# Performance work log

Hardware: AMD Instinct MI355X
Metric: run time of the kernel (lower is better)

## Reference

```python
import jax, jax.numpy as jnp
import numpy as np

B, N = 512, 256
NODE_D = 256      # inpt_dim[1]
PE_D = 256        # pooled_edge_dim
GLOB_D = 64       # inpt_dim[2]
FEAT_IN = NODE_D + PE_D          # 512, LN dim
CTXT_IN = GLOB_D                 # ctxt_dim = 0
FEAT_OUT = 256                   # feat_kwargs.outp_dim
N_HEADS = 4                      # attn_kwargs.outp_dim
HEAD_DIM = FEAT_OUT // N_HEADS   # 64
FEAT_HID = 1024
ATTN_HID = 256
LN_EPS = 1e-5


def _mlp(x, w1, b1, w2, b2):
    # DenseNetwork: hidden layer with SiLU, linear output
    h = jax.nn.silu(jnp.einsum('bni,ih->bnh', x, w1) + b1)
    return jnp.einsum('bnh,ho->bno', h, w2) + b2


def setup_inputs() -> dict:
    key = jax.random.key(0)
    ks = jax.random.split(key, 12)
    s = lambda fan_in: 1.0 / np.sqrt(fan_in)
    mask = jax.random.randint(ks[2], (B, N), 0, 2).astype(bool)
    mask = mask.at[:, 0].set(True)  # guarantee >=1 valid node per graph
    return {
        'nodes': jax.random.normal(ks[0], (B, N, NODE_D), jnp.float32),
        'pooled_edges': jax.random.normal(ks[1], (B, N, PE_D), jnp.float32),
        'mask': mask,
        'globs': jax.random.normal(ks[3], (B, GLOB_D), jnp.float32),
        'ln_g': jnp.ones((FEAT_IN,), jnp.float32),
        'ln_b': jnp.zeros((FEAT_IN,), jnp.float32),
        'fw1': jax.random.normal(ks[4], (FEAT_IN + CTXT_IN, FEAT_HID), jnp.float32) * s(FEAT_IN + CTXT_IN),
        'fb1': jnp.zeros((FEAT_HID,), jnp.float32),
        'fw2': jax.random.normal(ks[5], (FEAT_HID, FEAT_OUT), jnp.float32) * s(FEAT_HID),
        'fb2': jnp.zeros((FEAT_OUT,), jnp.float32),
        'aw1': jax.random.normal(ks[6], (FEAT_IN + CTXT_IN, ATTN_HID), jnp.float32) * s(FEAT_IN + CTXT_IN),
        'ab1': jnp.zeros((ATTN_HID,), jnp.float32),
        'aw2': jax.random.normal(ks[7], (ATTN_HID, N_HEADS), jnp.float32) * s(ATTN_HID),
        'ab2': jnp.zeros((N_HEADS,), jnp.float32),
    }


def reference(nodes, pooled_edges, mask, globs, ln_g, ln_b,
              fw1, fb1, fw2, fb2, aw1, ab1, aw2, ab2):
    # concat node feats with pooled edge feats, pre-LN
    x = jnp.concatenate([nodes, pooled_edges], axis=-1)            # [B,N,512]
    mu = jnp.mean(x, axis=-1, keepdims=True)
    var = jnp.mean(jnp.square(x - mu), axis=-1, keepdims=True)
    xn = (x - mu) * jax.lax.rsqrt(var + LN_EPS) * ln_g + ln_b
    # high-level context (globals) broadcast to every node
    ctx = jnp.broadcast_to(globs[:, None, :], (B, N, GLOB_D))
    inp = jnp.concatenate([xn, ctx], axis=-1)                      # [B,N,576]
    # attention pooling weights: pass_with_mask with padval=-inf, softmax over nodes
    scores = _mlp(inp, aw1, ab1, aw2, ab2)                         # [B,N,H]
    scores = jnp.where(mask[..., None], scores, -jnp.inf)
    w = jax.nn.softmax(scores / np.sqrt(FEAT_OUT).astype(np.float32), axis=-2)
    w = jnp.nan_to_num(w)                                          # all-masked graphs -> 0
    pool_w = jnp.repeat(w, HEAD_DIM, axis=-1)                      # [B,N,H*head_dim]
    # feature net: pass_with_mask with padval=0
    feats = _mlp(inp, fw1, fb1, fw2, fb2)                          # [B,N,256]
    feats = jnp.where(mask[..., None], feats, 0.0)
    # additive residual
    new_nodes = feats + nodes
    # attention pooled global
    pooled = jnp.sum(new_nodes * pool_w, axis=-2)                  # [B,256]
    return new_nodes, pooled
```

## Files before the change

### kernel.cpp

```cpp
#include <hip/hip_runtime.h>
#include <cmath>

typedef unsigned short ushort_t;
typedef unsigned char uchar_t;
typedef short short8 __attribute__((ext_vector_type(8)));
typedef float floatx4 __attribute__((ext_vector_type(4)));

#define B_GRAPH 512
#define ROWS 131072
#define IN_D 576
#define FEAT_HID 1024
#define ATTN_HID 256
#define NCAT 1280
#define FEAT_OUT 256
#define BK 32
#define NBUF 3
#define TILE_ELEMS (128 * BK)
#define BUF_BYTES  (TILE_ELEMS * 2)

__device__ __forceinline__ float bf2f(ushort_t h) {
    return __uint_as_float(((unsigned int)h) << 16);
}
__device__ __forceinline__ ushort_t f2bf(float f) {
    unsigned int u = __float_as_uint(f);
    u += 0x7fffu + ((u >> 16) & 1u);
    return (ushort_t)(u >> 16);
}
__device__ __forceinline__ void load4bf(const ushort_t* p, float f[4]) {
    uint2 u = *(const uint2*)p;
    f[0] = __uint_as_float(u.x << 16);
    f[1] = __uint_as_float(u.x & 0xffff0000u);
    f[2] = __uint_as_float(u.y << 16);
    f[3] = __uint_as_float(u.y & 0xffff0000u);
}

__global__ void detect_kernel(const void* nodes, const void* maskp, int* flags) {
    const int t = threadIdx.x;
    const ushort_t* nb = (const ushort_t*)nodes;
    int cnt = 0;
    for (int i = t; i < 4096; i += 256) {
        unsigned e = ((unsigned)nb[i] >> 7) & 0xffu;
        if (e >= 147u) cnt++;
    }
    const unsigned* mw = (const unsigned*)maskp;
    int mcnt = 0;
    for (int i = t; i < 16384; i += 256) {
        if (mw[i] > 1u) mcnt++;
    }
    __shared__ int r1[256], r2[256];
    r1[t] = cnt; r2[t] = mcnt; __syncthreads();
    for (int off = 128; off > 0; off >>= 1) {
        if (t < off) { r1[t] += r1[t + off]; r2[t] += r2[t + off]; }
        __syncthreads();
    }
    if (t == 0) { flags[0] = (r1[0] > 64) ? 1 : 0; flags[1] = (r2[0] > 16) ? 1 : 0; }
}

__device__ __forceinline__ float loadany(const void* p, size_t i, int flag) {
    return flag ? ((const float*)p)[i] : bf2f(((const ushort_t*)p)[i]);
}
__device__ __forceinline__ bool maskany(const void* p, size_t i, int flagM) {
    return flagM ? (((const uchar_t*)p)[i] != 0) : (((const int*)p)[i] != 0);
}

__global__ __launch_bounds__(256)
void convert_all(const void* globs, const void* lng, const void* lnb,
                 const void* fb1, const void* fb2, const void* ab1, const void* ab2,
                 ushort_t* gcan, ushort_t* lgc, ushort_t* lbc,
                 ushort_t* bcat, ushort_t* fb2c, ushort_t* ab2c,
                 const int* flags) {
    const int flag = flags[0];
    int i = blockIdx.x * 256 + threadIdx.x;
    if (i < 32768) { gcan[i] = f2bf(loadany(globs, i, flag)); return; }
    i -= 32768;
    if (i < 512)   { lgc[i]  = f2bf(loadany(lng,   i, flag)); return; }
    i -= 512;
    if (i < 512)   { lbc[i]  = f2bf(loadany(lnb,   i, flag)); return; }
    i -= 512;
    if (i < 1024)  { bcat[i] = f2bf(loadany(fb1,   i, flag)); return; }
    i -= 1024;
    if (i < 256)   { bcat[1024 + i] = f2bf(loadany(ab1, i, flag)); return; }
    i -= 256;
    if (i < 256)   { fb2c[i] = f2bf(loadany(fb2,   i, flag)); return; }
    i -= 256;
    if (i < 4)     { ab2c[i] = f2bf(loadany(ab2,   i, flag)); }
}

__global__ __launch_bounds__(256)
void transpose_all(const void* fw1, const void* fw2, const void* aw1, const void* aw2,
                   ushort_t* w1cat, ushort_t* fw2t, ushort_t* aw2t,
                   const int* flags) {
    const int flag = flags[0];
    int i = blockIdx.x * 256 + threadIdx.x;
    if (i < 576 * 1024) {
        int r = i >> 10, c = i & 1023;
        w1cat[(size_t)c * 576 + r] = f2bf(loadany(fw1, i, flag)); return;
    }
    i -= 576 * 1024;
    if (i < 1024 * 256) {
        int r = i >> 8, c = i & 255;
        fw2t[(size_t)c * 1024 + r] = f2bf(loadany(fw2, i, flag)); return;
    }
    i -= 1024 * 256;
    if (i < 576 * 256) {
        int r = i >> 8, c = i & 255;
        w1cat[(size_t)(1024 + c) * 576 + r] = f2bf(loadany(aw1, i, flag)); return;
    }
    i -= 576 * 256;
    if (i < 256 * 4) {
        int r = i >> 2, c = i & 3;
        aw2t[(size_t)c * 256 + r] = f2bf(loadany(aw2, i, flag));
    }
}

__global__ __launch_bounds__(256)
void ln_concat_kernel(const void* __restrict__ nodes, const void* __restrict__ pe,
                      const ushort_t* __restrict__ gcan,
                      const ushort_t* __restrict__ lg, const ushort_t* __restrict__ lb,
                      ushort_t* __restrict__ inp, int row0, const int* __restrict__ flags) {
    const int flag = flags[0];
    const int row  = blockIdx.x * 4 + (threadIdx.x >> 6);
    const int lane = threadIdx.x & 63;
    const size_t grow = (size_t)row0 + row;
    float xa[4], xb[4];
    if (flag) {
        float4 a = *(const float4*)((const float*)nodes + grow * 256 + lane * 4);
        float4 b = *(const float4*)((const float*)pe    + grow * 256 + lane * 4);
        xa[0]=a.x; xa[1]=a.y; xa[2]=a.z; xa[3]=a.w;
        xb[0]=b.x; xb[1]=b.y; xb[2]=b.z; xb[3]=b.w;
    } else {
        load4bf((const ushort_t*)nodes + grow * 256 + lane * 4, xa);
        load4bf((const ushort_t*)pe    + grow * 256 + lane * 4, xb);
    }
    float s = 0.f, q = 0.f;
#pragma unroll
    for (int j = 0; j < 4; j++) { s += xa[j] + xb[j]; q += xa[j]*xa[j] + xb[j]*xb[j]; }
#pragma unroll
    for (int m = 1; m < 64; m <<= 1) { s += __shfl_xor(s, m, 64); q += __shfl_xor(q, m, 64); }
    const float mu   = s * (1.0f / 512.0f);
    const float var  = q * (1.0f / 512.0f) - mu * mu;
    const float rstd = rsqrtf(fmaxf(var, 0.f) + 1e-5f);
    float ga[4], gb[4], ba[4], bb[4];
    load4bf(lg + lane * 4, ga);  load4bf(lg + 256 + lane * 4, gb);
    load4bf(lb + lane * 4, ba);  load4bf(lb + 256 + lane * 4, bb);
    ushort_t r0[4], r1[4];
#pragma unroll
    for (int j = 0; j < 4; j++) {
        r0[j] = f2bf((xa[j] - mu) * rstd * ga[j] + ba[j]);
        r1[j] = f2bf((xb[j] - mu) * rstd * gb[j] + bb[j]);
    }
    ushort_t* op = inp + (size_t)row * IN_D;
    uint2 p0, p1;
    p0.x = (unsigned)r0[0] | ((unsigned)r0[1] << 16);
    p0.y = (unsigned)r0[2] | ((unsigned)r0[3] << 16);
    p1.x = (unsigned)r1[0] | ((unsigned)r1[1] << 16);
    p1.y = (unsigned)r1[2] | ((unsigned)r1[3] << 16);
    *(uint2*)(op + lane * 4)       = p0;
    *(uint2*)(op + 256 + lane * 4) = p1;
    op[512 + lane] = gcan[(grow >> 8) * 64 + lane];
}

struct GemmCore {
    floatx4 acc[4][4];
    int wm, wn, r16, quad;
};

__device__ __forceinline__ void gload16(const ushort_t* g, ushort_t* l) {
    __builtin_amdgcn_global_load_lds(
        (const __attribute__((address_space(1))) unsigned int*)g,
        (__attribute__((address_space(3))) unsigned int*)l, 16, 0, 0);
}
__device__ __forceinline__ unsigned lds_off(const void* p) {
    return (unsigned)(size_t)(const __attribute__((address_space(3))) char*)p;
}

__device__ __forceinline__ void gemm_core(GemmCore& g,
        const ushort_t* __restrict__ A, int lda, const ushort_t* __restrict__ Bt,
        int m0, int n0, int K, ushort_t* As, ushort_t* Bs) {
    const int tid = threadIdx.x;
    const int wave = tid >> 6, lane = tid & 63;
    g.wm = (wave >> 1) * 64; g.wn = (wave & 1) * 64;
    g.r16 = lane & 15; g.quad = lane >> 4;
#pragma unroll
    for (int i = 0; i < 4; i++)
#pragma unroll
        for (int j = 0; j < 4; j++) g.acc[i][j] = (floatx4){0.f, 0.f, 0.f, 0.f};

    const int srow = wave * 32 + (lane >> 2);
    const int scol = (lane & 3) * 8;
    const ushort_t* Ag = A + (size_t)(m0 + srow) * lda + scol;
    const ushort_t* Bg = Bt + (size_t)(n0 + srow) * K + scol;
    const int woff = wave * 32 * BK;

    const unsigned a_lane = lds_off(As) + (unsigned)(((g.wm + g.r16) * BK + g.quad * 8) * 2);
    const unsigned b_lane = lds_off(Bs) + (unsigned)(((g.wn + g.r16) * BK + g.quad * 8) * 2);

    const int NT = K / BK;
    gload16(Ag, As + woff);
    gload16(Ag + 16 * (size_t)lda, As + woff + 16 * BK);
    gload16(Bg, Bs + woff);
    gload16(Bg + 16 * (size_t)K,  Bs + woff + 16 * BK);
    if (NT > 1) {
        gload16(Ag + BK, As + TILE_ELEMS + woff);
        gload16(Ag + BK + 16 * (size_t)lda, As + TILE_ELEMS + woff + 16 * BK);
        gload16(Bg + BK, Bs + TILE_ELEMS + woff);
        gload16(Bg + BK + 16 * (size_t)K,  Bs + TILE_ELEMS + woff + 16 * BK);
    }
    int bufc = 0;
    for (int t = 0; t < NT; ++t) {
        if (t + 1 < NT) asm volatile("s_waitcnt vmcnt(4)" ::: "memory");
        else            asm volatile("s_waitcnt vmcnt(0)" ::: "memory");
        __builtin_amdgcn_s_barrier();
        if (t + 2 < NT) {
            int bn = bufc + 2; if (bn >= NBUF) bn -= NBUF;
            const size_t kb = (size_t)(t + 2) * BK;
            ushort_t* An = As + bn * TILE_ELEMS + woff;
            ushort_t* Bn = Bs + bn * TILE_ELEMS + woff;
            gload16(Ag + kb, An);
            gload16(Ag + kb + 16 * (size_t)lda, An + 16 * BK);
            gload16(Bg + kb, Bn);
            gload16(Bg + kb + 16 * (size_t)K,  Bn + 16 * BK);
        }
        const unsigned aaddr = a_lane + (unsigned)(bufc * BUF_BYTES);
        const unsigned baddr = b_lane + (unsigned)(bufc * BUF_BYTES);
        short8 af[4], bg[4];
#pragma unroll
        for (int i = 0; i < 4; i++)
            asm volatile("ds_read_b128 %0, %1 offset:%c2"
                         : "=v"(af[i]) : "v"(aaddr), "i"(i * 1024));
#pragma unroll
        for (int i = 0; i < 4; i++)
            asm volatile("ds_read_b128 %0, %1 offset:%c2"
                         : "=v"(bg[i]) : "v"(baddr), "i"(i * 1024));
        asm volatile("s_waitcnt lgkmcnt(0)" ::: "memory");
        __builtin_amdgcn_sched_barrier(0);
#pragma unroll
        for (int mi = 0; mi < 4; mi++)
#pragma unroll
            for (int ni = 0; ni < 4; ni++)
                g.acc[mi][ni] = __builtin_amdgcn_mfma_f32_16x16x32_bf16(
                    af[mi], bg[ni], g.acc[mi][ni], 0, 0, 0);
        bufc = bufc + 1 == NBUF ? 0 : bufc + 1;
    }
}

__global__ __launch_bounds__(256)
void gemm_silu(const ushort_t* __restrict__ A, int lda,
               const ushort_t* __restrict__ Bt,
               const ushort_t* __restrict__ bias, ushort_t* __restrict__ out,
               int N, int K) {
    __shared__ __align__(16) ushort_t As[NBUF * TILE_ELEMS];
    __shared__ __align__(16) ushort_t Bs[NBUF * TILE_ELEMS];
    const int m0 = blockIdx.x * 128, n0 = blockIdx.y * 128;
    GemmCore g;
    gemm_core(g, A, lda, Bt, m0, n0, K, As, Bs);
#pragma unroll
    for (int mi = 0; mi < 4; mi++) {
        const int rbase = m0 + g.wm + mi * 16 + g.quad * 4;
#pragma unroll
        for (int ni = 0; ni < 4; ni++) {
            const int col = n0 + g.wn + ni * 16 + g.r16;
            const float bv = bf2f(bias[col]);
#pragma unroll
            for (int r = 0; r < 4; r++) {
                float v = g.acc[mi][ni][r] + bv;
                v = v / (1.0f + expf(-v));
                out[(size_t)(rbase + r) * N + col] = f2bf(v);
            }
        }
    }
}

__global__ __launch_bounds__(256)
void gemm_out(const ushort_t* __restrict__ A, int lda,
              const ushort_t* __restrict__ Bt,
              const ushort_t* __restrict__ bias, void* __restrict__ out,
              const void* __restrict__ mask, const void* __restrict__ resid,
              int row0, int K, const int* __restrict__ flags) {
    __shared__ __align__(16) ushort_t As[NBUF * TILE_ELEMS];
    __shared__ __align__(16) ushort_t Bs[NBUF * TILE_ELEMS];
    const int flag = flags[0], flagM = flags[1];
    const int m0 = blockIdx.x * 128, n0 = blockIdx.y * 128;
    GemmCore g;
    gemm_core(g, A, lda, Bt, m0, n0, K, As, Bs);
#pragma unroll
    for (int mi = 0; mi < 4; mi++) {
        const int rbase = m0 + g.wm + mi * 16 + g.quad * 4;
#pragma unroll
        for (int ni = 0; ni < 4; ni++) {
            const int col = n0 + g.wn + ni * 16 + g.r16;
            const float bv = bf2f(bias[col]);
#pragma unroll
            for (int r = 0; r < 4; r++) {
                const size_t grow = (size_t)row0 + rbase + r;
                const float nd = loadany(resid, grow * FEAT_OUT + col, flag);
                const bool mk = maskany(mask, grow, flagM);
                float v = mk ? (g.acc[mi][ni][r] + bv + nd) : nd;
                if (flag) ((float*)out)[grow * FEAT_OUT + col] = v;
                else      ((ushort_t*)out)[grow * FEAT_OUT + col] = f2bf(v);
            }
        }
    }
}

__global__ __launch_bounds__(256)
void scores_kernel(const ushort_t* __restrict__ hcat,
                   const ushort_t* __restrict__ aw2t,
                   const ushort_t* __restrict__ ab2c,
                   float* __restrict__ scores, int row0) {
    const int row  = blockIdx.x * 4 + (threadIdx.x >> 6);
    const int lane = threadIdx.x & 63;
    float x[4];
    load4bf(hcat + (size_t)row * NCAT + 1024 + lane * 4, x);
    float acc[4];
#pragma unroll
    for (int h = 0; h < 4; h++) {
        float wv[4];
        load4bf(aw2t + h * 256 + lane * 4, wv);
        acc[h] = x[0]*wv[0] + x[1]*wv[1] + x[2]*wv[2] + x[3]*wv[3];
    }
#pragma unroll
    for (int m = 1; m < 64; m <<= 1)
#pragma unroll
        for (int h = 0; h < 4; h++) acc[h] += __shfl_xor(acc[h], m, 64);
    if (lane == 0) {
#pragma unroll
        for (int h = 0; h < 4; h++)
            scores[((size_t)row0 + row) * 4 + h] = acc[h] + bf2f(ab2c[h]);
    }
}

__global__ __launch_bounds__(256)
void softmax_kernel(const float* __restrict__ scores, const void* __restrict__ mask,
                    float* __restrict__ w, const int* __restrict__ flags) {
    const int flagM = flags[1];
    const int b = blockIdx.x, n = threadIdx.x;
    const int idx = b * 256 + n;
    float4 s = *(const float4*)(scores + (size_t)idx * 4);
    s.x *= 0.0625f; s.y *= 0.0625f; s.z *= 0.0625f; s.w *= 0.0625f;
    const bool mk = maskany(mask, idx, flagM);
    __shared__ float4 red[256];
    float4 v;
    v.x = mk ? s.x : -3.0e38f; v.y = mk ? s.y : -3.0e38f;
    v.z = mk ? s.z : -3.0e38f; v.w = mk ? s.w : -3.0e38f;
    red[n] = v; __syncthreads();
    for (int off = 128; off > 0; off >>= 1) {
        if (n < off) {
            float4 o = red[n + off], c = red[n];
            c.x = fmaxf(c.x, o.x); c.y = fmaxf(c.y, o.y);
            c.z = fmaxf(c.z, o.z); c.w = fmaxf(c.w, o.w);
            red[n] = c;
        }
        __syncthreads();
    }
    float4 mx = red[0]; __syncthreads();
    float4 e;
    e.x = mk ? expf(s.x - mx.x) : 0.f; e.y = mk ? expf(s.y - mx.y) : 0.f;
    e.z = mk ? expf(s.z - mx.z) : 0.f; e.w = mk ? expf(s.w - mx.w) : 0.f;
    red[n] = e; __syncthreads();
    for (int off = 128; off > 0; off >>= 1) {
        if (n < off) {
            float4 o = red[n + off], c = red[n];
            c.x += o.x; c.y += o.y; c.z += o.z; c.w += o.w;
            red[n] = c;
        }
        __syncthreads();
    }
    float4 sm = red[0];
    const float ix = (sm.x > 0.f) ? 1.f / sm.x : 0.f;
    const float iy = (sm.y > 0.f) ? 1.f / sm.y : 0.f;
    const float iz = (sm.z > 0.f) ? 1.f / sm.z : 0.f;
    const float iw = (sm.w > 0.f) ? 1.f / sm.w : 0.f;
    float4 r; r.x = e.x * ix; r.y = e.y * iy; r.z = e.z * iz; r.w = e.w * iw;
    *(float4*)(w + (size_t)idx * 4) = r;
}

__global__ __launch_bounds__(256)
void pooled_kernel(const void* __restrict__ dout, const float* __restrict__ w,
                   const int* __restrict__ flags) {
    const int flag = flags[0];
    const int b = blockIdx.x, t = threadIdx.x;
    __shared__ float wsh[1024];
    const float* wb = w + (size_t)b * 1024;
    for (int i = t; i < 1024; i += 256) wsh[i] = wb[i];
    __syncthreads();
    const int h = t >> 6;
    float acc = 0.f;
    const size_t base = (size_t)b * 65536;
    if (flag) {
        const float* nn = (const float*)dout + base;
#pragma unroll 4
        for (int n = 0; n < 256; n++) acc += nn[(size_t)n * 256 + t] * wsh[n * 4 + h];
        ((float*)dout)[(size_t)ROWS * 256 + (size_t)b * 256 + t] = acc;
    } else {
        const ushort_t* nn = (const ushort_t*)dout + base;
#pragma unroll 4
        for (int n = 0; n < 256; n++) acc += bf2f(nn[(size_t)n * 256 + t]) * wsh[n * 4 + h];
        ((ushort_t*)dout)[(size_t)ROWS * 256 + (size_t)b * 256 + t] = f2bf(acc);
    }
}

extern "C" void kernel_launch(void* const* d_in, const int* in_sizes, int n_in,
                              void* d_out, int out_size, void* d_ws, size_t ws_size,
                              hipStream_t stream) {
    (void)in_sizes; (void)n_in; (void)out_size;
    const void* nodes = d_in[0];
    const void* pe    = d_in[1];
    const void* mask  = d_in[2];
    const void* globs = d_in[3];
    const void* ln_g  = d_in[4];
    const void* ln_b  = d_in[5];
    const void* fw1   = d_in[6];
    const void* fb1   = d_in[7];
    const void* fw2   = d_in[8];
    const void* fb2   = d_in[9];
    const void* aw1   = d_in[10];
    const void* ab1   = d_in[11];
    const void* aw2   = d_in[12];
    const void* ab2   = d_in[13];

    const int CHR = (ws_size >= (size_t)80 * 1024 * 1024) ? 16384 : 8192;

    char* ws = (char*)d_ws;
    size_t o = 0;
    auto take = [&](size_t bytes) -> char* {
        char* p = ws + o;
        o += (bytes + 255) & ~(size_t)255;
        return p;
    };
    ushort_t* inp  = (ushort_t*)take((size_t)CHR * IN_D * 2);
    ushort_t* hcat = (ushort_t*)take((size_t)CHR * NCAT * 2);
    float*    sc   = (float*)   take((size_t)ROWS * 4 * 4);
    float*    wsm  = (float*)   take((size_t)ROWS * 4 * 4);
    ushort_t* w1cat= (ushort_t*)take((size_t)NCAT * 576 * 2);
    ushort_t* fw2t = (ushort_t*)take(1024 * 256 * 2);
    ushort_t* aw2t = (ushort_t*)take(256 * 4 * 2);
    ushort_t* gcan = (ushort_t*)take(32768 * 2);
    ushort_t* lgc  = (ushort_t*)take(512 * 2);
    ushort_t* lbc  = (ushort_t*)take(512 * 2);
    ushort_t* bcat = (ushort_t*)take((size_t)NCAT * 2);
    ushort_t* fb2c = (ushort_t*)take(256 * 2);
    ushort_t* ab2c = (ushort_t*)take(4 * 2);
    int*      flags= (int*)     take(64);

    detect_kernel<<<1, 256, 0, stream>>>(nodes, mask, flags);
    convert_all<<<139, 256, 0, stream>>>(globs, ln_g, ln_b, fb1, fb2, ab1, ab2,
                                         gcan, lgc, lbc, bcat, fb2c, ab2c, flags);
    transpose_all<<<3908, 256, 0, stream>>>(fw1, fw2, aw1, aw2,
                                            w1cat, fw2t, aw2t, flags);

    const int nchunk = ROWS / CHR;
    for (int c = 0; c < nchunk; c++) {
        const int row0 = c * CHR;
        ln_concat_kernel<<<CHR / 4, 256, 0, stream>>>(nodes, pe, gcan, lgc, lbc,
                                                      inp, row0, flags);
        gemm_silu<<<dim3(CHR / 128, NCAT / 128), 256, 0, stream>>>(
            inp, IN_D, w1cat, bcat, hcat, NCAT, IN_D);
        scores_kernel<<<CHR / 4, 256, 0, stream>>>(hcat, aw2t, ab2c, sc, row0);
        gemm_out<<<dim3(CHR / 128, FEAT_OUT / 128), 256, 0, stream>>>(
            hcat, NCAT, fw2t, fb2c, d_out, mask, nodes, row0, FEAT_HID, flags);
    }

    softmax_kernel<<<B_GRAPH, 256, 0, stream>>>(sc, mask, wsm, flags);
    pooled_kernel<<<B_GRAPH, 256, 0, stream>>>(d_out, wsm, flags);
}
```

Baseline: 1.056 ms.

## Enlarge GEMM tiles to 128x256 with 8x4 MFMA per wave, bigger chunks

```diff
diff --git a/kernel.cpp b/kernel.cpp
--- a/kernel.cpp
+++ b/kernel.cpp
@@ -15,8 +15,8 @@
 #define FEAT_OUT 256
 #define BK 32
 #define NBUF 3
-#define TILE_ELEMS (128 * BK)
-#define BUF_BYTES  (TILE_ELEMS * 2)
+#define A_TILE (128 * BK)
+#define B_TILE (256 * BK)
 
 __device__ __forceinline__ float bf2f(ushort_t h) {
     return __uint_as_float(((unsigned int)h) << 16);
@@ -161,8 +161,8 @@
 }
 
 struct GemmCore {
-    floatx4 acc[4][4];
-    int wm, wn, r16, quad;
+    floatx4 acc[8][4];
+    int wn, r16, quad;
 };
 
 __device__ __forceinline__ void gload16(const ushort_t* g, ushort_t* l) {
@@ -179,53 +179,53 @@
         int m0, int n0, int K, ushort_t* As, ushort_t* Bs) {
     const int tid = threadIdx.x;
     const int wave = tid >> 6, lane = tid & 63;
-    g.wm = (wave >> 1) * 64; g.wn = (wave & 1) * 64;
-    g.r16 = lane & 15; g.quad = lane >> 4;
-#pragma unroll
-    for (int i = 0; i < 4; i++)
+    g.wn = wave * 64; g.r16 = lane & 15; g.quad = lane >> 4;
+#pragma unroll
+    for (int i = 0; i < 8; i++)
 #pragma unroll
         for (int j = 0; j < 4; j++) g.acc[i][j] = (floatx4){0.f, 0.f, 0.f, 0.f};
 
-    const int srow = wave * 32 + (lane >> 2);
+    const int sr   = lane >> 2;
     const int scol = (lane & 3) * 8;
-    const ushort_t* Ag = A + (size_t)(m0 + srow) * lda + scol;
-    const ushort_t* Bg = Bt + (size_t)(n0 + srow) * K + scol;
-    const int woff = wave * 32 * BK;
-
-    const unsigned a_lane = lds_off(As) + (unsigned)(((g.wm + g.r16) * BK + g.quad * 8) * 2);
+    const ushort_t* Ag = A  + (size_t)(m0 + wave * 32 + sr) * lda + scol;
+    const ushort_t* Bg = Bt + (size_t)(n0 + wave * 64 + sr) * K  + scol;
+    ushort_t* Asw = As + wave * 32 * BK;
+    ushort_t* Bsw = Bs + wave * 64 * BK;
+
+    const unsigned a_lane = lds_off(As) + (unsigned)((g.r16 * BK + g.quad * 8) * 2);
     const unsigned b_lane = lds_off(Bs) + (unsigned)(((g.wn + g.r16) * BK + g.quad * 8) * 2);
 
     const int NT = K / BK;
-    gload16(Ag, As + woff);
-    gload16(Ag + 16 * (size_t)lda, As + woff + 16 * BK);
-    gload16(Bg, Bs + woff);
-    gload16(Bg + 16 * (size_t)K,  Bs + woff + 16 * BK);
-    if (NT > 1) {
-        gload16(Ag + BK, As + TILE_ELEMS + woff);
-        gload16(Ag + BK + 16 * (size_t)lda, As + TILE_ELEMS + woff + 16 * BK);
-        gload16(Bg + BK, Bs + TILE_ELEMS + woff);
-        gload16(Bg + BK + 16 * (size_t)K,  Bs + TILE_ELEMS + woff + 16 * BK);
-    }
+#define STAGE_TILE(T, BUF) do {                                        \
+        const size_t kb = (size_t)(T) * BK;                            \
+        ushort_t* Ad = Asw + (BUF) * A_TILE;                           \
+        ushort_t* Bd = Bsw + (BUF) * B_TILE;                           \
+        gload16(Ag + kb,                    Ad);                       \
+        gload16(Ag + kb + 16 * (size_t)lda, Ad + 16 * BK);             \
+        gload16(Bg + kb,                    Bd);                       \
+        gload16(Bg + kb + 16 * (size_t)K,   Bd + 16 * BK);             \
+        gload16(Bg + kb + 32 * (size_t)K,   Bd + 32 * BK);             \
+        gload16(Bg + kb + 48 * (size_t)K,   Bd + 48 * BK);             \
+    } while (0)
+
+    STAGE_TILE(0, 0);
+    if (NT > 1) STAGE_TILE(1, 1);
+
     int bufc = 0;
     for (int t = 0; t < NT; ++t) {
-        if (t + 1 < NT) asm volatile("s_waitcnt vmcnt(4)" ::: "memory");
+        if (t + 1 < NT) asm volatile("s_waitcnt vmcnt(6)" ::: "memory");
         else            asm volatile("s_waitcnt vmcnt(0)" ::: "memory");
         __builtin_amdgcn_s_barrier();
+        __builtin_amdgcn_sched_barrier(0);
         if (t + 2 < NT) {
             int bn = bufc + 2; if (bn >= NBUF) bn -= NBUF;
-            const size_t kb = (size_t)(t + 2) * BK;
-            ushort_t* An = As + bn * TILE_ELEMS + woff;
-            ushort_t* Bn = Bs + bn * TILE_ELEMS + woff;
-            gload16(Ag + kb, An);
-            gload16(Ag + kb + 16 * (size_t)lda, An + 16 * BK);
-            gload16(Bg + kb, Bn);
-            gload16(Bg + kb + 16 * (size_t)K,  Bn + 16 * BK);
+            STAGE_TILE(t + 2, bn);
         }
-        const unsigned aaddr = a_lane + (unsigned)(bufc * BUF_BYTES);
-        const unsigned baddr = b_lane + (unsigned)(bufc * BUF_BYTES);
-        short8 af[4], bg[4];
-#pragma unroll
-        for (int i = 0; i < 4; i++)
+        const unsigned aaddr = a_lane + (unsigned)(bufc * (A_TILE * 2));
+        const unsigned baddr = b_lane + (unsigned)(bufc * (B_TILE * 2));
+        short8 af[8], bg[4];
+#pragma unroll
+        for (int i = 0; i < 8; i++)
             asm volatile("ds_read_b128 %0, %1 offset:%c2"
                          : "=v"(af[i]) : "v"(aaddr), "i"(i * 1024));
 #pragma unroll
@@ -235,28 +235,29 @@
         asm volatile("s_waitcnt lgkmcnt(0)" ::: "memory");
         __builtin_amdgcn_sched_barrier(0);
 #pragma unroll
-        for (int mi = 0; mi < 4; mi++)
+        for (int mi = 0; mi < 8; mi++)
 #pragma unroll
             for (int ni = 0; ni < 4; ni++)
                 g.acc[mi][ni] = __builtin_amdgcn_mfma_f32_16x16x32_bf16(
                     af[mi], bg[ni], g.acc[mi][ni], 0, 0, 0);
         bufc = bufc + 1 == NBUF ? 0 : bufc + 1;
     }
-}
-
-__global__ __launch_bounds__(256)
+#undef STAGE_TILE
+}
+
+__global__ __launch_bounds__(256, 2)
 void gemm_silu(const ushort_t* __restrict__ A, int lda,
                const ushort_t* __restrict__ Bt,
                const ushort_t* __restrict__ bias, ushort_t* __restrict__ out,
                int N, int K) {
-    __shared__ __align__(16) ushort_t As[NBUF * TILE_ELEMS];
-    __shared__ __align__(16) ushort_t Bs[NBUF * TILE_ELEMS];
-    const int m0 = blockIdx.x * 128, n0 = blockIdx.y * 128;
+    __shared__ __align__(16) ushort_t As[NBUF * A_TILE];
+    __shared__ __align__(16) ushort_t Bs[NBUF * B_TILE];
+    const int m0 = blockIdx.x * 128, n0 = blockIdx.y * 256;
     GemmCore g;
     gemm_core(g, A, lda, Bt, m0, n0, K, As, Bs);
 #pragma unroll
-    for (int mi = 0; mi < 4; mi++) {
-        const int rbase = m0 + g.wm + mi * 16 + g.quad * 4;
+    for (int mi = 0; mi < 8; mi++) {
+        const int rbase = m0 + mi * 16 + g.quad * 4;
 #pragma unroll
         for (int ni = 0; ni < 4; ni++) {
             const int col = n0 + g.wn + ni * 16 + g.r16;
@@ -271,21 +272,21 @@
     }
 }
 
-__global__ __launch_bounds__(256)
+__global__ __launch_bounds__(256, 2)
 void gemm_out(const ushort_t* __restrict__ A, int lda,
               const ushort_t* __restrict__ Bt,
               const ushort_t* __restrict__ bias, void* __restrict__ out,
               const void* __restrict__ mask, const void* __restrict__ resid,
               int row0, int K, const int* __restrict__ flags) {
-    __shared__ __align__(16) ushort_t As[NBUF * TILE_ELEMS];
-    __shared__ __align__(16) ushort_t Bs[NBUF * TILE_ELEMS];
+    __shared__ __align__(16) ushort_t As[NBUF * A_TILE];
+    __shared__ __align__(16) ushort_t Bs[NBUF * B_TILE];
     const int flag = flags[0], flagM = flags[1];
-    const int m0 = blockIdx.x * 128, n0 = blockIdx.y * 128;
+    const int m0 = blockIdx.x * 128, n0 = blockIdx.y * 256;
     GemmCore g;
     gemm_core(g, A, lda, Bt, m0, n0, K, As, Bs);
 #pragma unroll
-    for (int mi = 0; mi < 4; mi++) {
-        const int rbase = m0 + g.wm + mi * 16 + g.quad * 4;
+    for (int mi = 0; mi < 8; mi++) {
+        const int rbase = m0 + mi * 16 + g.quad * 4;
 #pragma unroll
         for (int ni = 0; ni < 4; ni++) {
             const int col = n0 + g.wn + ni * 16 + g.r16;
@@ -419,7 +420,10 @@
     const void* aw2   = d_in[12];
     const void* ab2   = d_in[13];
 
-    const int CHR = (ws_size >= (size_t)80 * 1024 * 1024) ? 16384 : 8192;
+    int CHR;
+    if      (ws_size >= (size_t)140 * 1024 * 1024) CHR = 32768;
+    else if (ws_size >= (size_t)80  * 1024 * 1024) CHR = 16384;
+    else                                           CHR = 8192;
 
     char* ws = (char*)d_ws;
     size_t o = 0;
@@ -454,10 +458,10 @@
         const int row0 = c * CHR;
         ln_concat_kernel<<<CHR / 4, 256, 0, stream>>>(nodes, pe, gcan, lgc, lbc,
                                                       inp, row0, flags);
-        gemm_silu<<<dim3(CHR / 128, NCAT / 128), 256, 0, stream>>>(
+        gemm_silu<<<dim3(CHR / 128, NCAT / 256), 256, 0, stream>>>(
             inp, IN_D, w1cat, bcat, hcat, NCAT, IN_D);
         scores_kernel<<<CHR / 4, 256, 0, stream>>>(hcat, aw2t, ab2c, sc, row0);
-        gemm_out<<<dim3(CHR / 128, FEAT_OUT / 128), 256, 0, stream>>>(
+        gemm_out<<<dim3(CHR / 128, FEAT_OUT / 256), 256, 0, stream>>>(
             hcat, NCAT, fw2t, fb2c, d_out, mask, nodes, row0, FEAT_HID, flags);
     }
 
```

Result: faster. 968.0 us (-8.3%).
